# Kernel tuning notes

Measured on AMD Instinct MI355X. Metric: run time of the kernel, lower is better.

The kernel has to match this reference:

```python
import jax, jax.numpy as jnp
import numpy as np
from jax import lax


def ternarize(w):
    """Standard TWN ternarization with straight-through estimator.
    delta = 0.7*mean(|w|); alpha = mean(|w|) over kept entries; w_t = alpha*sign(w)*mask.
    """
    a = jnp.abs(w)
    delta = 0.7 * a.mean()
    mask = (a > delta).astype(w.dtype)
    alpha = (a * mask).sum() / jnp.maximum(mask.sum(), 1.0)
    wt = alpha * jnp.sign(w) * mask
    return w + lax.stop_gradient(wt - w)  # STE


def conv3x3(x, w, b):
    y = lax.conv_general_dilated(x, ternarize(w), window_strides=(1, 1),
                                 padding=((1, 1), (1, 1)),
                                 dimension_numbers=('NCHW', 'OIHW', 'NCHW'))
    return y + b[None, :, None, None]


def maxpool2(x):
    return lax.reduce_window(x, -jnp.inf, lax.max, (1, 1, 2, 2), (1, 1, 2, 2), 'VALID')


def setup_inputs() -> dict:
    key = jax.random.key(0)
    ks = jax.random.split(key, 11)
    s = lambda k, shape, scale: jax.random.normal(k, shape, dtype=jnp.float32) * scale
    return {
        'x':   s(ks[0], (1024, 3, 32, 32), 1.0),
        'w1':  s(ks[1], (64, 3, 3, 3), 0.1),
        'b1':  s(ks[2], (64,), 0.01),
        'w2':  s(ks[3], (128, 64, 3, 3), 0.05),
        'b2':  s(ks[4], (128,), 0.01),
        'w3':  s(ks[5], (256, 128, 3, 3), 0.03),
        'b3':  s(ks[6], (256,), 0.01),
        'wf1': s(ks[7], (256, 4096), 0.02),
        'bf1': s(ks[8], (256,), 0.01),
        'wf2': s(ks[9], (10, 256), 0.06),
        'bf2': s(ks[10], (10,), 0.01),
    }


def reference(x, w1, b1, w2, b2, w3, b3, wf1, bf1, wf2, bf2):
    x = maxpool2(jax.nn.relu(conv3x3(x, w1, b1)))   # [B,64,16,16]
    x = maxpool2(jax.nn.relu(conv3x3(x, w2, b2)))   # [B,128,8,8]
    x = maxpool2(jax.nn.relu(conv3x3(x, w3, b3)))   # [B,256,4,4]
    x = x.reshape(-1, 256 * 4 * 4)
    x = jax.nn.relu(x @ ternarize(wf1).T + bf1)     # [B,256]
    return x @ ternarize(wf2).T + bf2               # [B,10]
```

## Files before the change

### kernel.cpp

```cpp
#include <hip/hip_runtime.h>
#include <hip/hip_bf16.h>


typedef __attribute__((ext_vector_type(8))) short short8;
typedef __attribute__((ext_vector_type(4))) float f32x4;
typedef __attribute__((ext_vector_type(4))) int i32x4;

#define GLOAD_LDS16(g, l)                                              \
    __builtin_amdgcn_global_load_lds(                                  \
        (const __attribute__((address_space(1))) void*)(g),            \
        (__attribute__((address_space(3))) void*)(l), 16, 0, 0)

__device__ __forceinline__ unsigned short f2bf(float x) {
    unsigned u = __float_as_uint(x);
    return (unsigned short)((u + 0x7fffu + ((u >> 16) & 1u)) >> 16);
}
__device__ __forceinline__ float bf2f(unsigned short b) {
    return __uint_as_float(((unsigned)b) << 16);
}

__device__ __forceinline__ float calc_S1(const double* __restrict__ scr,
                                         float amaxx) {
    const int* ii = (const int*)(scr + 20);
    const double c2 = scr[2];
    const float alpha1 = (float)(scr[1] / (c2 > 1.0 ? c2 : 1.0));
    const float ub = alpha1 * (float)ii[3] * amaxx + __int_as_float(ii[6]);
    return 32512.0f / fmaxf(ub, 1e-30f);
}
__device__ __forceinline__ float calc_S2(const double* __restrict__ scr,
                                         float amax1) {
    const int* ii = (const int*)(scr + 20);
    const double c2 = scr[6];
    const float alpha2 = (float)(scr[5] / (c2 > 1.0 ? c2 : 1.0));
    const float ub = alpha2 * (float)ii[4] * amax1 + __int_as_float(ii[7]);
    return 32512.0f / fmaxf(ub, 1e-30f);
}
__device__ __forceinline__ float calc_S3(const double* __restrict__ scr,
                                         float amax2) {
    const int* ii = (const int*)(scr + 20);
    const double c2 = scr[10];
    const float alpha3 = (float)(scr[9] / (c2 > 1.0 ? c2 : 1.0));
    const float ub = alpha3 * (float)ii[5] * amax2 + __int_as_float(ii[8]);
    return 32512.0f / fmaxf(ub, 1e-30f);
}

#define WS_W1B   0
#define N_W1B    2048
#define WS_W2P   (WS_W1B + N_W1B)
#define N_W2P    (9*128*64)
#define WS_W3P   (WS_W2P + N_W2P)
#define N_W3P    (9*256*128)
#define WS_WTF1  (WS_W3P + N_W3P)
#define N_WTF1   (256*4096)
#define WS_WTF2  (WS_WTF1 + N_WTF1)
#define N_WTF2   (10*256)
#define WS_A1    (WS_WTF2 + N_WTF2)
#define N_A1     (1024*256*64)
#define WS_A2    (WS_A1 + N_A1)
#define N_A2     (1024*64*128)
#define WS_A3    (WS_A2 + N_A2)
#define N_A3     (1024*16*256)
#define WS_F1    (WS_A3 + N_A3)
#define N_F1     (1024*256)
#define WS_SCR   (WS_F1 + N_F1)

#define FC1_S    8

struct TernArgs {
    const float* w[6];
    int n[6];
};

__global__ void tern_stats1(TernArgs ta, double* __restrict__ scr) {
    const int wi = blockIdx.y;
    const float* __restrict__ w = ta.w[wi];
    const int n = ta.n[wi];
    __shared__ double red[4];
    const int lane = threadIdx.x & 63, wv = threadIdx.x >> 6;
    if (wi == 5) {
        float m = 0.f;
        for (int i = blockIdx.x * blockDim.x + threadIdx.x; i < n;
             i += gridDim.x * blockDim.x)
            m = fmaxf(m, fabsf(w[i]));
        #pragma unroll
        for (int off = 32; off > 0; off >>= 1)
            m = fmaxf(m, __shfl_down(m, off, 64));
        if (lane == 0) red[wv] = (double)m;
        __syncthreads();
        if (threadIdx.x == 0) {
            float mm = (float)fmax(fmax(red[0], red[1]), fmax(red[2], red[3]));
            atomicMax((int*)(scr + 20), __float_as_int(mm));
        }
        return;
    }
    double s = 0.0;
    for (int i = blockIdx.x * blockDim.x + threadIdx.x; i < n;
         i += gridDim.x * blockDim.x)
        s += (double)fabsf(w[i]);
    #pragma unroll
    for (int off = 32; off > 0; off >>= 1) s += __shfl_down(s, off, 64);
    if (lane == 0) red[wv] = s;
    __syncthreads();
    if (threadIdx.x == 0)
        atomicAdd(scr + wi * 4, red[0] + red[1] + red[2] + red[3]);
}

__global__ void tern_stats2(TernArgs ta,
                            const float* __restrict__ b1v,
                            const float* __restrict__ b2v,
                            const float* __restrict__ b3v,
                            signed char* __restrict__ w1b,
                            signed char* __restrict__ w2p8,
                            signed char* __restrict__ w3p8,
                            signed char* __restrict__ wtf1b8,
                            signed char* __restrict__ wtf2b8,
                            double* __restrict__ scr) {
    const int wi = blockIdx.y;
    const int lane = threadIdx.x & 63, wv = threadIdx.x >> 6;

    if (wi == 5) {
        int* ii = (int*)(scr + 20);
        const int gw = blockIdx.x * 4 + wv;
        if (gw < 64) {
            const float d = (float)(0.7 * scr[0] / 1728.0);
            const float* row = ta.w[0] + gw * 27;
            int c = (lane < 27) ? (fabsf(row[lane]) > d ? 1 : 0) : 0;
            #pragma unroll
            for (int off = 32; off > 0; off >>= 1)
                c += __shfl_down(c, off, 64);
            if (lane == 0) atomicMax(ii + 3, c);
        } else if (gw < 192) {
            const float d = (float)(0.7 * scr[4] / 73728.0);
            const float* row = ta.w[1] + (long)(gw - 64) * 576;
            int c = 0;
            for (int k = lane; k < 576; k += 64)
                c += (fabsf(row[k]) > d) ? 1 : 0;
            #pragma unroll
            for (int off = 32; off > 0; off >>= 1)
                c += __shfl_down(c, off, 64);
            if (lane == 0) atomicMax(ii + 4, c);
        } else if (gw < 448) {
            const float d = (float)(0.7 * scr[8] / 294912.0);
            const float* row = ta.w[2] + (long)(gw - 192) * 1152;
            int c = 0;
            for (int k = lane; k < 1152; k += 64)
                c += (fabsf(row[k]) > d) ? 1 : 0;
            #pragma unroll
            for (int off = 32; off > 0; off >>= 1)
                c += __shfl_down(c, off, 64);
            if (lane == 0) atomicMax(ii + 5, c);
        } else if (gw < 451) {
            const float* bv = (gw == 448) ? b1v : (gw == 449) ? b2v : b3v;
            const int nb = (gw == 448) ? 64 : (gw == 449) ? 128 : 256;
            float m = 0.f;
            for (int k = lane; k < nb; k += 64) m = fmaxf(m, fabsf(bv[k]));
            #pragma unroll
            for (int off = 32; off > 0; off >>= 1)
                m = fmaxf(m, __shfl_down(m, off, 64));
            if (lane == 0)
                atomicMax(ii + 6 + (gw - 448), __float_as_int(m));
        }
        return;
    }

    const float* __restrict__ w = ta.w[wi];
    const int n = ta.n[wi];
    const float delta = (float)(0.7 * scr[wi * 4] / (double)n);

    if (wi == 0) {
        const int z0 = blockIdx.x * blockDim.x + threadIdx.x;
        const int zstride = gridDim.x * blockDim.x;
        for (int i = z0; i < 8192; i += zstride) {
            const int k = i & 63;
            const int plane = i >> 12;
            const bool sign_slot = plane == 0 ? (k < 27)
                                              : (k >= 32 && k < 59);
            if (!sign_slot) w1b[i] = 0;
        }
    }

    double ms = 0.0, cnt = 0.0;
    for (int i = blockIdx.x * blockDim.x + threadIdx.x; i < n;
         i += gridDim.x * blockDim.x) {
        const float v = w[i];
        const float a = fabsf(v);
        const bool mk = (a > delta);
        if (mk) { ms += (double)a; cnt += 1.0; }
        const signed char s = mk ? (v > 0.0f ? 1 : -1) : 0;
        if (wi == 0) {
            const int co = i / 27;
            const int kp = i % 27;
            w1b[co * 64 + kp] = s;
            w1b[4096 + co * 64 + 32 + kp] = s;
        } else if (wi == 1 || wi == 2) {
            const int CIc = (wi == 1) ? 64 : 128;
            const int COc = (wi == 1) ? 128 : 256;
            signed char* dst = (wi == 1) ? w2p8 : w3p8;
            const int co = i / (CIc * 9);
            const int r = i % (CIc * 9);
            const int ci = r / 9, tap = r % 9;
            dst[(tap * COc + co) * CIc + ci] = s;
        } else if (wi == 3) {
            const int j = i >> 12;
            const int k = i & 4095;
            const int px = k & 15, c = k >> 4;
            wtf1b8[(long)j * 4096 + px * 256 + c] = s;
        } else {
            wtf2b8[i] = s;
        }
    }
    #pragma unroll
    for (int off = 32; off > 0; off >>= 1) {
        ms += __shfl_down(ms, off, 64);
        cnt += __shfl_down(cnt, off, 64);
    }
    __shared__ double redm[4], redc[4];
    if (lane == 0) { redm[wv] = ms; redc[wv] = cnt; }
    __syncthreads();
    if (threadIdx.x == 0) {
        atomicAdd(scr + wi * 4 + 1, redm[0] + redm[1] + redm[2] + redm[3]);
        atomicAdd(scr + wi * 4 + 2, redc[0] + redc[1] + redc[2] + redc[3]);
    }
}

__global__ __launch_bounds__(256) void conv1_i8(
        const float* __restrict__ x,
        const signed char* __restrict__ w1b,
        const float* __restrict__ bias,
        const double* __restrict__ scr,
        const int* __restrict__ amax_x,
        int* __restrict__ amax_out,
        signed char* __restrict__ a1q) {
    constexpr int PL = 3472;
    __shared__ __align__(16) char X[2 * PL];
    __shared__ float redm[4];

    const int b = blockIdx.x;
    const int tid = threadIdx.x;
    const float amx = fmaxf(__int_as_float(*amax_x), 1e-30f);
    const float S = 32512.0f / amx;
    const float S1 = calc_S1(scr, __int_as_float(*amax_x));

    for (int i = tid; i < 2 * PL / 16; i += 256)
        ((int4*)X)[i] = make_int4(0, 0, 0, 0);
    __syncthreads();

    for (int i = tid; i < 768; i += 256) {
        const float4 v = ((const float4*)(x + (long)b * 3072))[i];
        const int e = i * 4;
        const int ci = e >> 10;
        const int rem = e & 1023;
        const int h = rem >> 5, w = rem & 31;
        const int base = ci * 1156 + (h + 1) * 34 + (w + 1);
        const float f[4] = {v.x, v.y, v.z, v.w};
        #pragma unroll
        for (int j = 0; j < 4; j++) {
            const int q = __float2int_rn(f[j] * S);
            const int ql = (q << 24) >> 24;
            const int qh = (q - ql) >> 8;
            X[base + j] = (char)ql;
            X[PL + base + j] = (char)qh;
        }
    }
    __syncthreads();

    const int lane = tid & 63;
    const int wid = tid >> 6;
    const int lm = lane & 15;
    const int kg = lane >> 4;

    const int poff = (kg >= 2) ? PL : 0;
    int cst[16];
    #pragma unroll
    for (int j = 0; j < 16; j++) {
        const int kp = (kg & 1) * 16 + j;
        cst[j] = (kp < 27)
                     ? ((kp / 9) * 1156 + ((kp % 9) / 3) * 34 + (kp % 9) % 3)
                     : 0;
    }

    i32x4 BL[4], BH[4];
    #pragma unroll
    for (int nt = 0; nt < 4; nt++) {
        const int co = nt * 16 + lm;
        BL[nt] = *(const i32x4*)(w1b + (long)co * 64 + kg * 16);
        BH[nt] = *(const i32x4*)(w1b + 4096 + (long)co * 64 + kg * 16);
    }

    const double c2 = scr[2];
    const float alpha = (float)(scr[1] / (c2 > 1.0 ? c2 : 1.0));
    const float dq = alpha / S;
    float tmax = 0.f;
    signed char* yb = a1q + (long)b * 32768;

    for (int tt = 0; tt < 16; ++tt) {
        const int t = wid * 16 + tt;
        const int pp = t * 4 + (lm >> 2);
        const int sub = lm & 3;
        const int h = 2 * (pp >> 4) + (sub >> 1);
        const int w = 2 * (pp & 15) + (sub & 1);
        const int base = poff + h * 34 + w;
        unsigned d[4] = {0u, 0u, 0u, 0u};
        #pragma unroll
        for (int j = 0; j < 16; j++) {
            const unsigned byte = (unsigned char)X[base + cst[j]];
            d[j >> 2] |= byte << ((j & 3) * 8);
        }
        i32x4 Af;
        Af[0] = (int)d[0]; Af[1] = (int)d[1];
        Af[2] = (int)d[2]; Af[3] = (int)d[3];

        const int opp = t * 4 + kg;
        const int ho = opp >> 4, wo = opp & 15;
        signed char* yrow = yb + ((long)ho * 2048) + wo * 64;
        #pragma unroll
        for (int nt = 0; nt < 4; nt++) {
            i32x4 aL = 0, aH = 0;
            aL = __builtin_amdgcn_mfma_i32_16x16x64_i8(Af, BL[nt], aL, 0, 0, 0);
            aH = __builtin_amdgcn_mfma_i32_16x16x64_i8(Af, BH[nt], aH, 0, 0, 0);
            const int s0 = aH[0] * 256 + aL[0];
            const int s1 = aH[1] * 256 + aL[1];
            const int s2 = aH[2] * 256 + aL[2];
            const int s3 = aH[3] * 256 + aL[3];
            int sm = s0 > s1 ? s0 : s1;
            const int sn = s2 > s3 ? s2 : s3;
            sm = sm > sn ? sm : sn;
            const int co = nt * 16 + lm;
            const float o = fmaxf(dq * (float)sm + bias[co], 0.f);
            tmax = fmaxf(tmax, o);
            const int q = (int)(o * S1 + 0.5f);
            const int ql = (q << 24) >> 24;
            const int qh = (q + 128) >> 8;
            const int slot = (nt + ((wo + 1) >> 1) + 2 * (ho + 1)) & 3;
            const int off = slot * 16 + lm;
            yrow[off] = (char)ql;
            yrow[1024 + off] = (char)qh;
        }
    }

    #pragma unroll
    for (int off = 32; off > 0; off >>= 1)
        tmax = fmaxf(tmax, __shfl_down(tmax, off, 64));
    if (lane == 0) redm[wid] = tmax;
    __syncthreads();
    if (tid == 0) {
        float m = fmaxf(fmaxf(redm[0], redm[1]), fmaxf(redm[2], redm[3]));
        atomicMax(amax_out, __float_as_int(m));
    }
}

template <int CI, int HI, int CO, int HB, int WM, int WN, int MODE, int WIDX>
__global__ __launch_bounds__(256, 2) void conv_i8(
        const signed char* __restrict__ xin,
        const signed char* __restrict__ wp,
        const float* __restrict__ bias,
        const double* __restrict__ scr,
        const int* __restrict__ amax_x,
        const int* __restrict__ amax_1,
        int* __restrict__ amax_2,
        void* __restrict__ yout) {
    constexpr int CH8 = CI / 64;
    constexpr int NITER = 9 * CH8;
    constexpr int HR = HI / HB;
    constexpr int ROWS = HR + 2;
    constexpr int COLS = HI + 2;
    constexpr int NPIX = ROWS * COLS;
    constexpr int PSTR = NPIX * 64 + 32;
    constexpr int PO = HI / 2;
    constexpr int POR = HR / 2;
    constexpr int MT = 4, NT = 4;
    constexpr int NPL = 2 * CH8;
    constexpr int RWQ = HI * 64 * 2;
    static_assert(WM * WN == 4, "4 waves");
    static_assert(WM * 64 == HR * HI, "M covers slab pixels");
    static_assert(WN * 64 == CO, "N covers all co");
    static_assert(MODE != 0 || (CI == 64 && RWQ == 2048), "conv2 shape");
    static_assert(MODE != 1 || (CI == 128 && HB == 1), "conv3 shape");
    static_assert(HB <= 2, "row compaction assumes <=1 invalid row per end");
    static_assert((COLS & 1) == 0, "swizzle parity uses even COLS");

    __shared__ __align__(16) char X[NPL * PSTR];
    __shared__ __align__(16) char RAW2[(MODE == 1) ? 16384 : 16];
    __shared__ float redm[4];

    const int bimg = blockIdx.x / HB;
    const int hb = blockIdx.x % HB;
    const int tid = threadIdx.x;
    const int lane = tid & 63;
    const int wid = tid >> 6;

    const float S_in = (MODE == 0)
                           ? calc_S1(scr, __int_as_float(*amax_x))
                           : calc_S2(scr, __int_as_float(*amax_1));

    const int rlo = (hb == 0) ? 1 : 0;
    const int rhi = (hb == HB - 1) ? (ROWS - 1) : ROWS;

    if (MODE == 0) {
        for (int r = rlo; r < rhi; r++) {
            #pragma unroll
            for (int pl = 0; pl < 2; pl++) {
                if (wid == ((r * 2 + pl) & 3)) {
                    const int h = hb * HR + r - 1;
                    const signed char* src = xin +
                        (long)(bimg * HI + h) * RWQ + pl * 1024 + lane * 16;
                    GLOAD_LDS16(src, &X[pl * PSTR + (r * COLS + 1) * 64]);
                }
            }
        }
    } else {
        #pragma unroll
        for (int j = 0; j < 16; j++) {
            if (wid == (j & 3)) {
                const signed char* src = xin + (long)bimg * 16384 +
                                         j * 1024 + lane * 16;
                GLOAD_LDS16(src, &RAW2[j * 1024]);
            }
        }
    }

    {
        const int nfull = ((hb == 0) ? 1 : 0) + ((hb == HB - 1) ? 1 : 0);
        const int NP1 = ROWS * 2;
        const int NPZ = NP1 + nfull * (COLS - 2);
        for (int i = tid; i < NPZ * NPL * 4; i += 256) {
            const int u = i & 3;
            const int t = i >> 2;
            const int g = t % NPL;
            const int e = t / NPL;
            int p;
            if (e < NP1) {
                const int row = e >> 1;
                p = row * COLS + ((e & 1) ? (COLS - 1) : 0);
            } else {
                const int e2 = e - NP1;
                const int inFirst = (hb == 0) && (e2 < COLS - 2);
                const int fr = inFirst ? 0 : (ROWS - 1);
                const int cc = inFirst ? e2
                                       : (e2 - ((hb == 0) ? (COLS - 2) : 0));
                p = fr * COLS + 1 + cc;
            }
            *(int4*)&X[g * PSTR + p * 64 + u * 16] = make_int4(0, 0, 0, 0);
        }
    }

    if (MODE == 1) {
        __syncthreads();
        #pragma unroll
        for (int k = 0; k < 16; k++) {
            const int v = tid + k * 256;
            const int h = v >> 9;
            const int r = v & 511;
            const int g = r >> 7;
            const int b4 = (r & 127) << 2;
            const unsigned d = *(const unsigned*)&RAW2[v << 2];
            *(unsigned*)&X[g * PSTR + ((h + 1) * COLS + 1) * 64 + b4] = d;
        }
    }
    __syncthreads();

    const int wm = (WM == 1) ? 0 : (wid >> 1);
    const int wn = (WM == 1) ? wid : (wid & 1);
    const int lm = lane & 15;
    const int kg = lane >> 4;

    int pq[MT];
    #pragma unroll
    for (int mt = 0; mt < MT; mt++) {
        const int m = (wm * MT + mt) * 16 + lm;
        const int pp = m >> 2, sub = m & 3;
        const int lph = pp / PO, lpw = pp % PO;
        const int h = 2 * lph + (sub >> 1);
        const int w = 2 * lpw + (sub & 1);
        pq[mt] = ((h * COLS + w) << 6) | ((h & 1) << 3) | (w & 7);
    }
    const signed char* bp[NT];
    #pragma unroll
    for (int nt = 0; nt < NT; nt++) {
        const int co = (wn * NT + nt) * 16 + lm;
        bp[nt] = wp + (long)co * CI + kg * 16;
    }

    i32x4 accL[MT][NT], accH[MT][NT];
    #pragma unroll
    for (int mt = 0; mt < MT; mt++)
        #pragma unroll
        for (int nt = 0; nt < NT; nt++) { accL[mt][nt] = 0; accH[mt][nt] = 0; }

    i32x4 Bb[2][NT];
    #pragma unroll
    for (int nt = 0; nt < NT; nt++) Bb[0][nt] = *(const i32x4*)(bp[nt]);

    #pragma unroll 2
    for (int it = 0; it < NITER; ++it) {
        const int cur = it & 1, nxt = cur ^ 1;
        if (it + 1 < NITER) {
            const int it1 = it + 1;
            const int tap = it1 / CH8, ch1 = it1 % CH8;
            const int woff = tap * CO * CI + ch1 * 64;
            #pragma unroll
            for (int nt = 0; nt < NT; nt++)
                Bb[nxt][nt] = *(const i32x4*)(bp[nt] + woff);
        }
        const int tap = it / CH8, ch = it % CH8;
        const int ty = tap / 3, tx = tap % 3;
        const int DT = (ty * COLS + tx) << 6;
        const int typ = ty & 1;
        int ao[MT];
        #pragma unroll
        for (int mt = 0; mt < MT; mt++) {
            const int q = pq[mt];
            const int slot = (kg + ((((q >> 3) & 1) + typ) & 1) * 2 +
                              (((q & 7) + tx) >> 1)) & 3;
            ao[mt] = (q & ~63) + DT + (slot << 4);
        }
        {
            i32x4 Af[MT];
            #pragma unroll
            for (int mt = 0; mt < MT; mt++)
                Af[mt] = *(const i32x4*)&X[ch * PSTR + ao[mt]];
            #pragma unroll
            for (int mt = 0; mt < MT; mt++)
                #pragma unroll
                for (int nt = 0; nt < NT; nt++)
                    accL[mt][nt] = __builtin_amdgcn_mfma_i32_16x16x64_i8(
                        Af[mt], Bb[cur][nt], accL[mt][nt], 0, 0, 0);
        }
        {
            i32x4 Af[MT];
            #pragma unroll
            for (int mt = 0; mt < MT; mt++)
                Af[mt] = *(const i32x4*)&X[(CH8 + ch) * PSTR + ao[mt]];
            #pragma unroll
            for (int mt = 0; mt < MT; mt++)
                #pragma unroll
                for (int nt = 0; nt < NT; nt++)
                    accH[mt][nt] = __builtin_amdgcn_mfma_i32_16x16x64_i8(
                        Af[mt], Bb[cur][nt], accH[mt][nt], 0, 0, 0);
        }
    }

    const double* wst = scr + WIDX * 4;
    const double c2 = wst[2];
    const float alpha = (float)(wst[1] / (c2 > 1.0 ? c2 : 1.0));
    const float dq = alpha / S_in;
    if (MODE == 0) {
        const float S2 = calc_S2(scr, __int_as_float(*amax_1));
        signed char* oq = (signed char*)yout;
        float tmax = 0.f;
        #pragma unroll
        for (int mt = 0; mt < MT; mt++) {
            const int pp = (wm * MT + mt) * 4 + kg;
            const int lph = pp / PO, lpw = pp % PO;
            const int h = hb * POR + lph;
            const int w = lpw;
            #pragma unroll
            for (int nt = 0; nt < NT; nt++) {
                const int co2 = (wn * NT + nt) * 16 + lm;
                const i32x4 aL = accL[mt][nt], aH = accH[mt][nt];
                int s0 = aH[0] * 256 + aL[0];
                int s1 = aH[1] * 256 + aL[1];
                int s2 = aH[2] * 256 + aL[2];
                int s3 = aH[3] * 256 + aL[3];
                int sm = s0 > s1 ? s0 : s1;
                int sn = s2 > s3 ? s2 : s3;
                sm = sm > sn ? sm : sn;
                const float o = fmaxf(dq * (float)sm + bias[co2], 0.f);
                tmax = fmaxf(tmax, o);
                const int q = (int)(o * S2 + 0.5f);
                const int ql = (q << 24) >> 24;
                const int qh = (q + 128) >> 8;
                const int slot = (((co2 >> 4) & 3) + ((w + 1) >> 1) +
                                  2 * (h + 1)) & 3;
                const long base = (long)bimg * 16384 + h * 2048 +
                                  (co2 >> 6) * 512 + w * 64 + slot * 16 +
                                  (co2 & 15);
                oq[base] = (char)ql;
                oq[base + 1024] = (char)qh;
            }
        }
        #pragma unroll
        for (int off = 32; off > 0; off >>= 1)
            tmax = fmaxf(tmax, __shfl_down(tmax, off, 64));
        if (lane == 0) redm[wid] = tmax;
        __syncthreads();
        if (tid == 0) {
            float m = fmaxf(fmaxf(redm[0], redm[1]), fmaxf(redm[2], redm[3]));
            atomicMax(amax_2, __float_as_int(m));
        }
    } else {
        const float S3 = calc_S3(scr, __int_as_float(*amax_2));
        signed char* oq = (signed char*)yout;
        #pragma unroll
        for (int mt = 0; mt < MT; mt++) {
            const int pp = (wm * MT + mt) * 4 + kg;
            const int lph = pp / PO, lpw = pp % PO;
            const int gpp = (hb * POR + lph) * PO + lpw;
            signed char* yr = oq + (long)bimg * 8192 + gpp * 512;
            #pragma unroll
            for (int nt = 0; nt < NT; nt++) {
                const int co = (wn * NT + nt) * 16 + lm;
                const i32x4 aL = accL[mt][nt], aH = accH[mt][nt];
                int s0 = aH[0] * 256 + aL[0];
                int s1 = aH[1] * 256 + aL[1];
                int s2 = aH[2] * 256 + aL[2];
                int s3 = aH[3] * 256 + aL[3];
                int sm = s0 > s1 ? s0 : s1;
                int sn = s2 > s3 ? s2 : s3;
                sm = sm > sn ? sm : sn;
                const float o = fmaxf(dq * (float)sm + bias[co], 0.f);
                const int q = (int)(o * S3 + 0.5f);
                const int ql = (q << 24) >> 24;
                const int qh = (q + 128) >> 8;
                yr[co] = (char)ql;
                yr[256 + co] = (char)qh;
            }
        }
    }
}

template <int S>
__global__ __launch_bounds__(256) void fc1_i8(
        const signed char* __restrict__ A,
        const signed char* __restrict__ Bw,
        float* __restrict__ parts) {
    constexpr int KCH = 4096 / S;
    constexpr int NCH = KCH / 64;
    const int m0 = blockIdx.x * 64;
    const int n0 = blockIdx.y * 64;
    const int s = blockIdx.z;
    const int tid = threadIdx.x;
    const int lane = tid & 63, wid = tid >> 6;
    const int wm = wid >> 1, wn = wid & 1;
    const int lm = lane & 15, kg = lane >> 4;

    const int k0 = s * KCH;
    const signed char* ap[2];
    const signed char* bp[2];
    #pragma unroll
    for (int t = 0; t < 2; t++) {
        ap[t] = A + (long)(m0 + wm * 32 + t * 16 + lm) * 8192;
        bp[t] = Bw + (long)(n0 + wn * 32 + t * 16 + lm) * 4096 + k0 + kg * 16;
    }

    i32x4 accL[2][2], accH[2][2];
    #pragma unroll
    for (int mt = 0; mt < 2; mt++)
        #pragma unroll
        for (int nt = 0; nt < 2; nt++) { accL[mt][nt] = 0; accH[mt][nt] = 0; }

    #pragma unroll
    for (int ch = 0; ch < NCH; ++ch) {
        const int kb = k0 + ch * 64;
        const int aoff = (kb >> 8) * 512 + (kb & 255) + kg * 16;
        i32x4 Ah[2], Al[2], Bb[2];
        #pragma unroll
        for (int t = 0; t < 2; t++) {
            Al[t] = *(const i32x4*)(ap[t] + aoff);
            Ah[t] = *(const i32x4*)(ap[t] + aoff + 256);
            Bb[t] = *(const i32x4*)(bp[t] + ch * 64);
        }
        #pragma unroll
        for (int mt = 0; mt < 2; mt++)
            #pragma unroll
            for (int nt = 0; nt < 2; nt++) {
                accH[mt][nt] = __builtin_amdgcn_mfma_i32_16x16x64_i8(
                    Ah[mt], Bb[nt], accH[mt][nt], 0, 0, 0);
                accL[mt][nt] = __builtin_amdgcn_mfma_i32_16x16x64_i8(
                    Al[mt], Bb[nt], accL[mt][nt], 0, 0, 0);
            }
    }

    #pragma unroll
    for (int mt = 0; mt < 2; mt++) {
        #pragma unroll
        for (int r = 0; r < 4; r++) {
            const int b = m0 + wm * 32 + mt * 16 + kg * 4 + r;
            #pragma unroll
            for (int nt = 0; nt < 2; nt++) {
                const int j = n0 + wn * 32 + nt * 16 + lm;
                const int sum = accH[mt][nt][r] * 256 + accL[mt][nt][r];
                parts[((long)s * 1024 + b) * 256 + j] = (float)sum;
            }
        }
    }
}

template <int S>
__global__ __launch_bounds__(256) void fc2_fused(
        const float* __restrict__ parts,
        const double* __restrict__ scr,
        const int* __restrict__ amax_2,
        const float* __restrict__ bf1v,
        const signed char* __restrict__ wtf2b8,
        const float* __restrict__ bf2v,
        float* __restrict__ out) {
    __shared__ float sf[256];
    const int b = blockIdx.x;
    const int j = threadIdx.x;
    float s = 0.f;
    #pragma unroll
    for (int p = 0; p < S; p++)
        s += parts[(long)p * 262144 + (long)b * 256 + j];
    const double c2 = scr[14];
    const float alpha = (float)(scr[13] / (c2 > 1.0 ? c2 : 1.0));
    const float S3 = calc_S3(scr, __int_as_float(*amax_2));
    sf[j] = fmaxf(alpha * s / S3 + bf1v[j], 0.f);
    __syncthreads();
    const double c4 = scr[18];
    const float alpha4 = (float)(scr[17] / (c4 > 1.0 ? c4 : 1.0));
    const int lane = threadIdx.x & 63, wid = threadIdx.x >> 6;
    for (int k = wid; k < 10; k += 4) {
        const signed char* wr = wtf2b8 + k * 256;
        float acc = 0.f;
        #pragma unroll
        for (int t = 0; t < 4; t++)
            acc += sf[lane + t * 64] * (float)wr[lane + t * 64];
        #pragma unroll
        for (int off = 32; off > 0; off >>= 1)
            acc += __shfl_down(acc, off, 64);
        if (lane == 0) out[(long)b * 10 + k] = acc * alpha4 + bf2v[k];
    }
}

extern "C" void kernel_launch(void* const* d_in, const int* in_sizes, int n_in,
                              void* d_out, int out_size, void* d_ws, size_t ws_size,
                              hipStream_t stream) {
    const float* x   = (const float*)d_in[0];
    const float* w1  = (const float*)d_in[1];
    const float* b1  = (const float*)d_in[2];
    const float* w2  = (const float*)d_in[3];
    const float* b2  = (const float*)d_in[4];
    const float* w3  = (const float*)d_in[5];
    const float* b3  = (const float*)d_in[6];
    const float* wf1 = (const float*)d_in[7];
    const float* bf1 = (const float*)d_in[8];
    const float* wf2 = (const float*)d_in[9];
    const float* bf2 = (const float*)d_in[10];
    float* out = (float*)d_out;
    float* ws = (float*)d_ws;

    const int B = 1024;

    signed char*    w1b    = (signed char*)(ws + WS_W1B);
    signed char*    w2p8   = (signed char*)(ws + WS_W2P);
    signed char*    w3p8   = (signed char*)(ws + WS_W3P);
    signed char*    wtf1b8 = (signed char*)(ws + WS_WTF1);
    signed char*    wtf2b8 = (signed char*)(ws + WS_WTF2);
    signed char*    a1q    = (signed char*)(ws + WS_A1);
    signed char*    a2q    = (signed char*)(ws + WS_A2);
    signed char*    a3q    = (signed char*)(ws + WS_A3);
    double*         scr    = (double*)(ws + WS_SCR);
    int*            iscr   = (int*)(scr + 20);
    int*            amaxx  = iscr;
    int*            amax1  = iscr + 1;
    int*            amax2  = iscr + 2;
    float*          parts  = ws + WS_A1;

    hipMemsetAsync(scr, 0, 26 * sizeof(double), stream);

    TernArgs ta;
    ta.w[0] = w1;  ta.n[0] = 64 * 27;
    ta.w[1] = w2;  ta.n[1] = 128 * 64 * 9;
    ta.w[2] = w3;  ta.n[2] = 256 * 128 * 9;
    ta.w[3] = wf1; ta.n[3] = 256 * 4096;
    ta.w[4] = wf2; ta.n[4] = 10 * 256;
    ta.w[5] = x;   ta.n[5] = 1024 * 3 * 32 * 32;

    hipLaunchKernelGGL(tern_stats1, dim3(128, 6), dim3(256), 0, stream, ta, scr);
    hipLaunchKernelGGL(tern_stats2, dim3(128, 6), dim3(256), 0, stream,
                       ta, b1, b2, b3, w1b, w2p8, w3p8, wtf1b8, wtf2b8, scr);

    hipLaunchKernelGGL(conv1_i8, dim3(B), dim3(256), 0, stream,
                       x, w1b, b1, scr, amaxx, amax1, a1q);

    hipLaunchKernelGGL((conv_i8<64, 16, 128, 2, 2, 2, 0, 1>), dim3(B * 2),
                       dim3(256), 0, stream, a1q, w2p8, b2, scr, amaxx,
                       amax1, amax2, a2q);

    hipLaunchKernelGGL((conv_i8<128, 8, 256, 1, 1, 4, 1, 2>), dim3(B),
                       dim3(256), 0, stream, a2q, w3p8, b3, scr, amaxx,
                       amax1, amax2, a3q);

    hipLaunchKernelGGL((fc1_i8<FC1_S>), dim3(16, 4, FC1_S), dim3(256), 0, stream,
                       a3q, wtf1b8, parts);

    hipLaunchKernelGGL((fc2_fused<FC1_S>), dim3(B), dim3(256), 0, stream,
                       parts, scr, amax2, bf1, wtf2b8, bf2, out);
}
```

Baseline: 261.1 us.

## Fuse conv1 and conv2 into one kernel keeping conv1 output in LDS

Merges the conv1 and conv2 kernels so each block computes the pooled conv1 output for one image straight into shared-memory slabs. Conv2 then runs over two row halves from LDS, so the int8 activation no longer makes a round trip through global memory and one launch is dropped. Because conv2's input scale now has to be known before the conv1 max is reduced, it is derived from an analytic bound (calc_S2b) rather than the measured conv1 max. That may coarsen quantization. The fused kernel uses more LDS per block and does conv2 with half the blocks of before, which could reduce occupancy and parallelism.

```diff
diff --git a/kernel.cpp b/kernel.cpp
--- a/kernel.cpp
+++ b/kernel.cpp
@@ -27,13 +27,16 @@
     const float ub = alpha1 * (float)ii[3] * amaxx + __int_as_float(ii[6]);
     return 32512.0f / fmaxf(ub, 1e-30f);
 }
-__device__ __forceinline__ float calc_S2(const double* __restrict__ scr,
-                                         float amax1) {
+__device__ __forceinline__ float calc_S2b(const double* __restrict__ scr,
+                                          float amaxx) {
     const int* ii = (const int*)(scr + 20);
+    const double c1 = scr[2];
+    const float alpha1 = (float)(scr[1] / (c1 > 1.0 ? c1 : 1.0));
+    const float ub1 = alpha1 * (float)ii[3] * amaxx + __int_as_float(ii[6]);
     const double c2 = scr[6];
     const float alpha2 = (float)(scr[5] / (c2 > 1.0 ? c2 : 1.0));
-    const float ub = alpha2 * (float)ii[4] * amax1 + __int_as_float(ii[7]);
-    return 32512.0f / fmaxf(ub, 1e-30f);
+    const float ub2 = alpha2 * (float)ii[4] * ub1 + __int_as_float(ii[7]);
+    return 32512.0f / fmaxf(ub2, 1e-30f);
 }
 __device__ __forceinline__ float calc_S3(const double* __restrict__ scr,
                                          float amax2) {
@@ -223,26 +226,58 @@
     }
 }
 
-__global__ __launch_bounds__(256) void conv1_i8(
+__global__ __launch_bounds__(256, 2) void conv12_i8(
         const float* __restrict__ x,
         const signed char* __restrict__ w1b,
-        const float* __restrict__ bias,
+        const float* __restrict__ b1v,
+        const signed char* __restrict__ w2p,
+        const float* __restrict__ b2v,
         const double* __restrict__ scr,
         const int* __restrict__ amax_x,
-        int* __restrict__ amax_out,
-        signed char* __restrict__ a1q) {
+        int* __restrict__ amax_2,
+        signed char* __restrict__ a2q) {
     constexpr int PL = 3472;
-    __shared__ __align__(16) char X[2 * PL];
-    __shared__ float redm[4];
+    constexpr int COLS = 18;
+    constexpr int PSTR2 = 180 * 64 + 32;
+    constexpr int SLAB = 2 * PSTR2;
+    constexpr int PO = 8, POR = 4;
+    constexpr int MT = 4, NT = 4, CI = 64, CO = 128;
+
+    __shared__ __align__(16) char XA[2 * PL];
+    __shared__ __align__(16) char X2[2 * SLAB];
+    __shared__ float redt[4];
 
     const int b = blockIdx.x;
     const int tid = threadIdx.x;
+    const int lane = tid & 63, wid = tid >> 6;
+    const int lm = lane & 15, kg = lane >> 4;
+
     const float amx = fmaxf(__int_as_float(*amax_x), 1e-30f);
     const float S = 32512.0f / amx;
     const float S1 = calc_S1(scr, __int_as_float(*amax_x));
 
+    if (tid < 4) redt[tid] = 0.f;
     for (int i = tid; i < 2 * PL / 16; i += 256)
-        ((int4*)X)[i] = make_int4(0, 0, 0, 0);
+        ((int4*)XA)[i] = make_int4(0, 0, 0, 0);
+    for (int i = tid; i < 2 * 36 * 2 * 4; i += 256) {
+        const int u = i & 3;
+        const int t = i >> 2;
+        const int g = t & 1;
+        const int e = t >> 1;
+        const int slab = e / 36;
+        const int k = e % 36;
+        int p;
+        if (slab == 0)
+            p = (k < 18) ? k
+                         : ((1 + ((k - 18) >> 1)) * COLS +
+                            (((k - 18) & 1) ? (COLS - 1) : 0));
+        else
+            p = (k < 18) ? (9 * COLS + k)
+                         : ((((k - 18) >> 1)) * COLS +
+                            (((k - 18) & 1) ? (COLS - 1) : 0));
+        *(int4*)&X2[slab * SLAB + g * PSTR2 + p * 64 + u * 16] =
+            make_int4(0, 0, 0, 0);
+    }
     __syncthreads();
 
     for (int i = tid; i < 768; i += 256) {
@@ -258,212 +293,95 @@
             const int q = __float2int_rn(f[j] * S);
             const int ql = (q << 24) >> 24;
             const int qh = (q - ql) >> 8;
-            X[base + j] = (char)ql;
-            X[PL + base + j] = (char)qh;
+            XA[base + j] = (char)ql;
+            XA[PL + base + j] = (char)qh;
         }
     }
     __syncthreads();
 
-    const int lane = tid & 63;
-    const int wid = tid >> 6;
-    const int lm = lane & 15;
-    const int kg = lane >> 4;
-
-    const int poff = (kg >= 2) ? PL : 0;
-    int cst[16];
-    #pragma unroll
-    for (int j = 0; j < 16; j++) {
-        const int kp = (kg & 1) * 16 + j;
-        cst[j] = (kp < 27)
-                     ? ((kp / 9) * 1156 + ((kp % 9) / 3) * 34 + (kp % 9) % 3)
-                     : 0;
-    }
-
-    i32x4 BL[4], BH[4];
-    #pragma unroll
-    for (int nt = 0; nt < 4; nt++) {
-        const int co = nt * 16 + lm;
-        BL[nt] = *(const i32x4*)(w1b + (long)co * 64 + kg * 16);
-        BH[nt] = *(const i32x4*)(w1b + 4096 + (long)co * 64 + kg * 16);
-    }
-
-    const double c2 = scr[2];
-    const float alpha = (float)(scr[1] / (c2 > 1.0 ? c2 : 1.0));
-    const float dq = alpha / S;
-    float tmax = 0.f;
-    signed char* yb = a1q + (long)b * 32768;
-
-    for (int tt = 0; tt < 16; ++tt) {
-        const int t = wid * 16 + tt;
-        const int pp = t * 4 + (lm >> 2);
-        const int sub = lm & 3;
-        const int h = 2 * (pp >> 4) + (sub >> 1);
-        const int w = 2 * (pp & 15) + (sub & 1);
-        const int base = poff + h * 34 + w;
-        unsigned d[4] = {0u, 0u, 0u, 0u};
+    {
+        const int poff = (kg >= 2) ? PL : 0;
+        int cst[16];
         #pragma unroll
         for (int j = 0; j < 16; j++) {
-            const unsigned byte = (unsigned char)X[base + cst[j]];
-            d[j >> 2] |= byte << ((j & 3) * 8);
-        }
-        i32x4 Af;
-        Af[0] = (int)d[0]; Af[1] = (int)d[1];
-        Af[2] = (int)d[2]; Af[3] = (int)d[3];
-
-        const int opp = t * 4 + kg;
-        const int ho = opp >> 4, wo = opp & 15;
-        signed char* yrow = yb + ((long)ho * 2048) + wo * 64;
+            const int kp = (kg & 1) * 16 + j;
+            cst[j] = (kp < 27)
+                         ? ((kp / 9) * 1156 + ((kp % 9) / 3) * 34 +
+                            (kp % 9) % 3)
+                         : 0;
+        }
+        i32x4 BL[4], BH[4];
         #pragma unroll
         for (int nt = 0; nt < 4; nt++) {
-            i32x4 aL = 0, aH = 0;
-            aL = __builtin_amdgcn_mfma_i32_16x16x64_i8(Af, BL[nt], aL, 0, 0, 0);
-            aH = __builtin_amdgcn_mfma_i32_16x16x64_i8(Af, BH[nt], aH, 0, 0, 0);
-            const int s0 = aH[0] * 256 + aL[0];
-            const int s1 = aH[1] * 256 + aL[1];
-            const int s2 = aH[2] * 256 + aL[2];
-            const int s3 = aH[3] * 256 + aL[3];
-            int sm = s0 > s1 ? s0 : s1;
-            const int sn = s2 > s3 ? s2 : s3;
-            sm = sm > sn ? sm : sn;
             const int co = nt * 16 + lm;
-            const float o = fmaxf(dq * (float)sm + bias[co], 0.f);
-            tmax = fmaxf(tmax, o);
-            const int q = (int)(o * S1 + 0.5f);
-            const int ql = (q << 24) >> 24;
-            const int qh = (q + 128) >> 8;
-            const int slot = (nt + ((wo + 1) >> 1) + 2 * (ho + 1)) & 3;
-            const int off = slot * 16 + lm;
-            yrow[off] = (char)ql;
-            yrow[1024 + off] = (char)qh;
-        }
-    }
-
-    #pragma unroll
-    for (int off = 32; off > 0; off >>= 1)
-        tmax = fmaxf(tmax, __shfl_down(tmax, off, 64));
-    if (lane == 0) redm[wid] = tmax;
+            BL[nt] = *(const i32x4*)(w1b + (long)co * 64 + kg * 16);
+            BH[nt] = *(const i32x4*)(w1b + 4096 + (long)co * 64 + kg * 16);
+        }
+        const double c2a = scr[2];
+        const float alpha1 = (float)(scr[1] / (c2a > 1.0 ? c2a : 1.0));
+        const float dq1 = alpha1 / S;
+
+        for (int tt = 0; tt < 16; ++tt) {
+            const int t = wid * 16 + tt;
+            const int pp = t * 4 + (lm >> 2);
+            const int sub = lm & 3;
+            const int h = 2 * (pp >> 4) + (sub >> 1);
+            const int w = 2 * (pp & 15) + (sub & 1);
+            const int base = poff + h * 34 + w;
+            unsigned d[4] = {0u, 0u, 0u, 0u};
+            #pragma unroll
+            for (int j = 0; j < 16; j++) {
+                const unsigned byte = (unsigned char)XA[base + cst[j]];
+                d[j >> 2] |= byte << ((j & 3) * 8);
+            }
+            i32x4 Af;
+            Af[0] = (int)d[0]; Af[1] = (int)d[1];
+            Af[2] = (int)d[2]; Af[3] = (int)d[3];
+
+            const int opp = t * 4 + kg;
+            const int ho = opp >> 4, wo = opp & 15;
+            const int col = wo + 1;
+            #pragma unroll
+            for (int nt = 0; nt < 4; nt++) {
+                i32x4 aL = 0, aH = 0;
+                aL = __builtin_amdgcn_mfma_i32_16x16x64_i8(Af, BL[nt], aL,
+                                                           0, 0, 0);
+                aH = __builtin_amdgcn_mfma_i32_16x16x64_i8(Af, BH[nt], aH,
+                                                           0, 0, 0);
+                const int s0 = aH[0] * 256 + aL[0];
+                const int s1 = aH[1] * 256 + aL[1];
+                const int s2 = aH[2] * 256 + aL[2];
+                const int s3 = aH[3] * 256 + aL[3];
+                int sm = s0 > s1 ? s0 : s1;
+                const int sn = s2 > s3 ? s2 : s3;
+                sm = sm > sn ? sm : sn;
+                const int co = nt * 16 + lm;
+                const float o = fmaxf(dq1 * (float)sm + b1v[co], 0.f);
+                const int q = (int)(o * S1 + 0.5f);
+                const signed char ql = (signed char)((q << 24) >> 24);
+                const signed char qh = (signed char)((q + 128) >> 8);
+                const int sb = nt + (col >> 1);
+                if (ho <= 8) {
+                    const int r = ho + 1;
+                    const int slot = (sb + 2 * r) & 3;
+                    const int off = (r * COLS + col) * 64 + slot * 16 + lm;
+                    X2[off] = ql;
+                    X2[PSTR2 + off] = qh;
+                }
+                if (ho >= 7) {
+                    const int r = ho - 7;
+                    const int slot = (sb + 2 * r) & 3;
+                    const int off = (r * COLS + col) * 64 + slot * 16 + lm;
+                    X2[SLAB + off] = ql;
+                    X2[SLAB + PSTR2 + off] = qh;
+                }
+            }
+        }
+    }
     __syncthreads();
-    if (tid == 0) {
-        float m = fmaxf(fmaxf(redm[0], redm[1]), fmaxf(redm[2], redm[3]));
-        atomicMax(amax_out, __float_as_int(m));
-    }
-}
-
-template <int CI, int HI, int CO, int HB, int WM, int WN, int MODE, int WIDX>
-__global__ __launch_bounds__(256, 2) void conv_i8(
-        const signed char* __restrict__ xin,
-        const signed char* __restrict__ wp,
-        const float* __restrict__ bias,
-        const double* __restrict__ scr,
-        const int* __restrict__ amax_x,
-        const int* __restrict__ amax_1,
-        int* __restrict__ amax_2,
-        void* __restrict__ yout) {
-    constexpr int CH8 = CI / 64;
-    constexpr int NITER = 9 * CH8;
-    constexpr int HR = HI / HB;
-    constexpr int ROWS = HR + 2;
-    constexpr int COLS = HI + 2;
-    constexpr int NPIX = ROWS * COLS;
-    constexpr int PSTR = NPIX * 64 + 32;
-    constexpr int PO = HI / 2;
-    constexpr int POR = HR / 2;
-    constexpr int MT = 4, NT = 4;
-    constexpr int NPL = 2 * CH8;
-    constexpr int RWQ = HI * 64 * 2;
-    static_assert(WM * WN == 4, "4 waves");
-    static_assert(WM * 64 == HR * HI, "M covers slab pixels");
-    static_assert(WN * 64 == CO, "N covers all co");
-    static_assert(MODE != 0 || (CI == 64 && RWQ == 2048), "conv2 shape");
-    static_assert(MODE != 1 || (CI == 128 && HB == 1), "conv3 shape");
-    static_assert(HB <= 2, "row compaction assumes <=1 invalid row per end");
-    static_assert((COLS & 1) == 0, "swizzle parity uses even COLS");
-
-    __shared__ __align__(16) char X[NPL * PSTR];
-    __shared__ __align__(16) char RAW2[(MODE == 1) ? 16384 : 16];
-    __shared__ float redm[4];
-
-    const int bimg = blockIdx.x / HB;
-    const int hb = blockIdx.x % HB;
-    const int tid = threadIdx.x;
-    const int lane = tid & 63;
-    const int wid = tid >> 6;
-
-    const float S_in = (MODE == 0)
-                           ? calc_S1(scr, __int_as_float(*amax_x))
-                           : calc_S2(scr, __int_as_float(*amax_1));
-
-    const int rlo = (hb == 0) ? 1 : 0;
-    const int rhi = (hb == HB - 1) ? (ROWS - 1) : ROWS;
-
-    if (MODE == 0) {
-        for (int r = rlo; r < rhi; r++) {
-            #pragma unroll
-            for (int pl = 0; pl < 2; pl++) {
-                if (wid == ((r * 2 + pl) & 3)) {
-                    const int h = hb * HR + r - 1;
-                    const signed char* src = xin +
-                        (long)(bimg * HI + h) * RWQ + pl * 1024 + lane * 16;
-                    GLOAD_LDS16(src, &X[pl * PSTR + (r * COLS + 1) * 64]);
-                }
-            }
-        }
-    } else {
-        #pragma unroll
-        for (int j = 0; j < 16; j++) {
-            if (wid == (j & 3)) {
-                const signed char* src = xin + (long)bimg * 16384 +
-                                         j * 1024 + lane * 16;
-                GLOAD_LDS16(src, &RAW2[j * 1024]);
-            }
-        }
-    }
-
-    {
-        const int nfull = ((hb == 0) ? 1 : 0) + ((hb == HB - 1) ? 1 : 0);
-        const int NP1 = ROWS * 2;
-        const int NPZ = NP1 + nfull * (COLS - 2);
-        for (int i = tid; i < NPZ * NPL * 4; i += 256) {
-            const int u = i & 3;
-            const int t = i >> 2;
-            const int g = t % NPL;
-            const int e = t / NPL;
-            int p;
-            if (e < NP1) {
-                const int row = e >> 1;
-                p = row * COLS + ((e & 1) ? (COLS - 1) : 0);
-            } else {
-                const int e2 = e - NP1;
-                const int inFirst = (hb == 0) && (e2 < COLS - 2);
-                const int fr = inFirst ? 0 : (ROWS - 1);
-                const int cc = inFirst ? e2
-                                       : (e2 - ((hb == 0) ? (COLS - 2) : 0));
-                p = fr * COLS + 1 + cc;
-            }
-            *(int4*)&X[g * PSTR + p * 64 + u * 16] = make_int4(0, 0, 0, 0);
-        }
-    }
-
-    if (MODE == 1) {
-        __syncthreads();
-        #pragma unroll
-        for (int k = 0; k < 16; k++) {
-            const int v = tid + k * 256;
-            const int h = v >> 9;
-            const int r = v & 511;
-            const int g = r >> 7;
-            const int b4 = (r & 127) << 2;
-            const unsigned d = *(const unsigned*)&RAW2[v << 2];
-            *(unsigned*)&X[g * PSTR + ((h + 1) * COLS + 1) * 64 + b4] = d;
-        }
-    }
-    __syncthreads();
-
-    const int wm = (WM == 1) ? 0 : (wid >> 1);
-    const int wn = (WM == 1) ? wid : (wid & 1);
-    const int lm = lane & 15;
-    const int kg = lane >> 4;
-
+
+    const int wm = wid >> 1;
+    const int wn = wid & 1;
     int pq[MT];
     #pragma unroll
     for (int mt = 0; mt < MT; mt++) {
@@ -478,75 +396,73 @@
     #pragma unroll
     for (int nt = 0; nt < NT; nt++) {
         const int co = (wn * NT + nt) * 16 + lm;
-        bp[nt] = wp + (long)co * CI + kg * 16;
-    }
-
-    i32x4 accL[MT][NT], accH[MT][NT];
-    #pragma unroll
-    for (int mt = 0; mt < MT; mt++)
-        #pragma unroll
-        for (int nt = 0; nt < NT; nt++) { accL[mt][nt] = 0; accH[mt][nt] = 0; }
-
-    i32x4 Bb[2][NT];
-    #pragma unroll
-    for (int nt = 0; nt < NT; nt++) Bb[0][nt] = *(const i32x4*)(bp[nt]);
-
-    #pragma unroll 2
-    for (int it = 0; it < NITER; ++it) {
-        const int cur = it & 1, nxt = cur ^ 1;
-        if (it + 1 < NITER) {
-            const int it1 = it + 1;
-            const int tap = it1 / CH8, ch1 = it1 % CH8;
-            const int woff = tap * CO * CI + ch1 * 64;
-            #pragma unroll
-            for (int nt = 0; nt < NT; nt++)
-                Bb[nxt][nt] = *(const i32x4*)(bp[nt] + woff);
-        }
-        const int tap = it / CH8, ch = it % CH8;
-        const int ty = tap / 3, tx = tap % 3;
-        const int DT = (ty * COLS + tx) << 6;
-        const int typ = ty & 1;
-        int ao[MT];
-        #pragma unroll
-        for (int mt = 0; mt < MT; mt++) {
-            const int q = pq[mt];
-            const int slot = (kg + ((((q >> 3) & 1) + typ) & 1) * 2 +
-                              (((q & 7) + tx) >> 1)) & 3;
-            ao[mt] = (q & ~63) + DT + (slot << 4);
-        }
-        {
-            i32x4 Af[MT];
-            #pragma unroll
-            for (int mt = 0; mt < MT; mt++)
-                Af[mt] = *(const i32x4*)&X[ch * PSTR + ao[mt]];
-            #pragma unroll
-            for (int mt = 0; mt < MT; mt++)
+        bp[nt] = w2p + (long)co * CI + kg * 16;
+    }
+
+    for (int hb = 0; hb < 2; ++hb) {
+        const char* Xs = X2 + hb * SLAB;
+
+        i32x4 accL[MT][NT], accH[MT][NT];
+        #pragma unroll
+        for (int mt = 0; mt < MT; mt++)
+            #pragma unroll
+            for (int nt = 0; nt < NT; nt++) {
+                accL[mt][nt] = 0; accH[mt][nt] = 0;
+            }
+        i32x4 Bb[2][NT];
+        #pragma unroll
+        for (int nt = 0; nt < NT; nt++) Bb[0][nt] = *(const i32x4*)(bp[nt]);
+
+        #pragma unroll 2
+        for (int it = 0; it < 9; ++it) {
+            const int cur = it & 1, nxt = cur ^ 1;
+            if (it + 1 < 9) {
+                const int woff = (it + 1) * CO * CI;
                 #pragma unroll
                 for (int nt = 0; nt < NT; nt++)
-                    accL[mt][nt] = __builtin_amdgcn_mfma_i32_16x16x64_i8(
-                        Af[mt], Bb[cur][nt], accL[mt][nt], 0, 0, 0);
-        }
-        {
-            i32x4 Af[MT];
-            #pragma unroll
-            for (int mt = 0; mt < MT; mt++)
-                Af[mt] = *(const i32x4*)&X[(CH8 + ch) * PSTR + ao[mt]];
-            #pragma unroll
-            for (int mt = 0; mt < MT; mt++)
+                    Bb[nxt][nt] = *(const i32x4*)(bp[nt] + woff);
+            }
+            const int ty = it / 3, tx = it % 3;
+            const int DT = (ty * COLS + tx) << 6;
+            const int typ = ty & 1;
+            int ao[MT];
+            #pragma unroll
+            for (int mt = 0; mt < MT; mt++) {
+                const int q = pq[mt];
+                const int slot = (kg + ((((q >> 3) & 1) + typ) & 1) * 2 +
+                                  (((q & 7) + tx) >> 1)) & 3;
+                ao[mt] = (q & ~63) + DT + (slot << 4);
+            }
+            {
+                i32x4 Af[MT];
                 #pragma unroll
-                for (int nt = 0; nt < NT; nt++)
-                    accH[mt][nt] = __builtin_amdgcn_mfma_i32_16x16x64_i8(
-                        Af[mt], Bb[cur][nt], accH[mt][nt], 0, 0, 0);
-        }
-    }
-
-    const double* wst = scr + WIDX * 4;
-    const double c2 = wst[2];
-    const float alpha = (float)(wst[1] / (c2 > 1.0 ? c2 : 1.0));
-    const float dq = alpha / S_in;
-    if (MODE == 0) {
-        const float S2 = calc_S2(scr, __int_as_float(*amax_1));
-        signed char* oq = (signed char*)yout;
+                for (int mt = 0; mt < MT; mt++)
+                    Af[mt] = *(const i32x4*)&Xs[ao[mt]];
+                #pragma unroll
+                for (int mt = 0; mt < MT; mt++)
+                    #pragma unroll
+                    for (int nt = 0; nt < NT; nt++)
+                        accL[mt][nt] = __builtin_amdgcn_mfma_i32_16x16x64_i8(
+                            Af[mt], Bb[cur][nt], accL[mt][nt], 0, 0, 0);
+            }
+            {
+                i32x4 Af[MT];
+                #pragma unroll
+                for (int mt = 0; mt < MT; mt++)
+                    Af[mt] = *(const i32x4*)&Xs[PSTR2 + ao[mt]];
+                #pragma unroll
+                for (int mt = 0; mt < MT; mt++)
+                    #pragma unroll
+                    for (int nt = 0; nt < NT; nt++)
+                        accH[mt][nt] = __builtin_amdgcn_mfma_i32_16x16x64_i8(
+                            Af[mt], Bb[cur][nt], accH[mt][nt], 0, 0, 0);
+            }
+        }
+
+        const double c2b = scr[6];
+        const float alpha2 = (float)(scr[5] / (c2b > 1.0 ? c2b : 1.0));
+        const float dq2 = alpha2 / S1;
+        const float S2p = calc_S2b(scr, __int_as_float(*amax_x));
         float tmax = 0.f;
         #pragma unroll
         for (int mt = 0; mt < MT; mt++) {
@@ -565,56 +481,208 @@
                 int sm = s0 > s1 ? s0 : s1;
                 int sn = s2 > s3 ? s2 : s3;
                 sm = sm > sn ? sm : sn;
-                const float o = fmaxf(dq * (float)sm + bias[co2], 0.f);
+                const float o = fmaxf(dq2 * (float)sm + b2v[co2], 0.f);
                 tmax = fmaxf(tmax, o);
-                const int q = (int)(o * S2 + 0.5f);
+                const int q = (int)(o * S2p + 0.5f);
                 const int ql = (q << 24) >> 24;
                 const int qh = (q + 128) >> 8;
                 const int slot = (((co2 >> 4) & 3) + ((w + 1) >> 1) +
                                   2 * (h + 1)) & 3;
-                const long base = (long)bimg * 16384 + h * 2048 +
+                const long base = (long)b * 16384 + h * 2048 +
                                   (co2 >> 6) * 512 + w * 64 + slot * 16 +
                                   (co2 & 15);
-                oq[base] = (char)ql;
-                oq[base + 1024] = (char)qh;
+                a2q[base] = (char)ql;
+                a2q[base + 1024] = (char)qh;
             }
         }
         #pragma unroll
         for (int off = 32; off > 0; off >>= 1)
             tmax = fmaxf(tmax, __shfl_down(tmax, off, 64));
-        if (lane == 0) redm[wid] = tmax;
-        __syncthreads();
-        if (tid == 0) {
-            float m = fmaxf(fmaxf(redm[0], redm[1]), fmaxf(redm[2], redm[3]));
-            atomicMax(amax_2, __float_as_int(m));
-        }
-    } else {
-        const float S3 = calc_S3(scr, __int_as_float(*amax_2));
-        signed char* oq = (signed char*)yout;
+        if (lane == 0) redt[wid] = fmaxf(redt[wid], tmax);
+    }
+    __syncthreads();
+    if (tid == 0) {
+        float m = fmaxf(fmaxf(redt[0], redt[1]), fmaxf(redt[2], redt[3]));
+        atomicMax(amax_2, __float_as_int(m));
+    }
+}
+
+__global__ __launch_bounds__(256, 2) void conv3_i8(
+        const signed char* __restrict__ xin,
+        const signed char* __restrict__ wp,
+        const float* __restrict__ bias,
+        const double* __restrict__ scr,
+        const int* __restrict__ amax_x,
+        const int* __restrict__ amax_2,
+        signed char* __restrict__ a3q) {
+    constexpr int CI = 128, HI = 8, CO = 256;
+    constexpr int CH8 = CI / 64;
+    constexpr int NITER = 9 * CH8;
+    constexpr int ROWS = HI + 2, COLS = HI + 2;
+    constexpr int NPIX = ROWS * COLS;
+    constexpr int PSTR = NPIX * 64 + 32;
+    constexpr int PO = HI / 2;
+    constexpr int MT = 4, NT = 4;
+    constexpr int NPL = 2 * CH8;
+
+    __shared__ __align__(16) char X[NPL * PSTR];
+    __shared__ __align__(16) char RAW2[16384];
+
+    const int bimg = blockIdx.x;
+    const int tid = threadIdx.x;
+    const int lane = tid & 63;
+    const int wid = tid >> 6;
+
+    const float S_in = calc_S2b(scr, __int_as_float(*amax_x));
+
+    #pragma unroll
+    for (int j = 0; j < 16; j++) {
+        if (wid == (j & 3)) {
+            const signed char* src = xin + (long)bimg * 16384 +
+                                     j * 1024 + lane * 16;
+            GLOAD_LDS16(src, &RAW2[j * 1024]);
+        }
+    }
+
+    {
+        constexpr int NPZ = 2 * COLS + 2 * (ROWS - 2);
+        for (int i = tid; i < NPZ * NPL * 4; i += 256) {
+            const int u = i & 3;
+            const int t = i >> 2;
+            const int g = t % NPL;
+            const int e = t / NPL;
+            int p;
+            if (e < COLS) p = e;
+            else if (e < 2 * COLS) p = (ROWS - 1) * COLS + (e - COLS);
+            else {
+                const int e2 = e - 2 * COLS;
+                p = (1 + (e2 >> 1)) * COLS + ((e2 & 1) ? (COLS - 1) : 0);
+            }
+            *(int4*)&X[g * PSTR + p * 64 + u * 16] = make_int4(0, 0, 0, 0);
+        }
+    }
+
+    __syncthreads();
+    #pragma unroll
+    for (int k = 0; k < 16; k++) {
+        const int v = tid + k * 256;
+        const int h = v >> 9;
+        const int r = v & 511;
+        const int g = r >> 7;
+        const int b4 = (r & 127) << 2;
+        const unsigned d = *(const unsigned*)&RAW2[v << 2];
+        *(unsigned*)&X[g * PSTR + ((h + 1) * COLS + 1) * 64 + b4] = d;
+    }
+    __syncthreads();
+
+    const int wm = 0;
+    const int wn = wid;
+    const int lm = lane & 15;
+    const int kg = lane >> 4;
+
+    int pq[MT];
+    #pragma unroll
+    for (int mt = 0; mt < MT; mt++) {
+        const int m = (wm * MT + mt) * 16 + lm;
+        const int pp = m >> 2, sub = m & 3;
+        const int lph = pp / PO, lpw = pp % PO;
+        const int h = 2 * lph + (sub >> 1);
+        const int w = 2 * lpw + (sub & 1);
+        pq[mt] = ((h * COLS + w) << 6) | ((h & 1) << 3) | (w & 7);
+    }
+    const signed char* bp[NT];
+    #pragma unroll
+    for (int nt = 0; nt < NT; nt++) {
+        const int co = (wn * NT + nt) * 16 + lm;
+        bp[nt] = wp + (long)co * CI + kg * 16;
+    }
+
+    i32x4 accL[MT][NT], accH[MT][NT];
+    #pragma unroll
+    for (int mt = 0; mt < MT; mt++)
+        #pragma unroll
+        for (int nt = 0; nt < NT; nt++) { accL[mt][nt] = 0; accH[mt][nt] = 0; }
+
+    i32x4 Bb[2][NT];
+    #pragma unroll
+    for (int nt = 0; nt < NT; nt++) Bb[0][nt] = *(const i32x4*)(bp[nt]);
+
+    #pragma unroll 2
+    for (int it = 0; it < NITER; ++it) {
+        const int cur = it & 1, nxt = cur ^ 1;
+        if (it + 1 < NITER) {
+            const int it1 = it + 1;
+            const int tap = it1 / CH8, ch1 = it1 % CH8;
+            const int woff = tap * CO * CI + ch1 * 64;
+            #pragma unroll
+            for (int nt = 0; nt < NT; nt++)
+                Bb[nxt][nt] = *(const i32x4*)(bp[nt] + woff);
+        }
+        const int tap = it / CH8, ch = it % CH8;
+        const int ty = tap / 3, tx = tap % 3;
+        const int DT = (ty * COLS + tx) << 6;
+        const int typ = ty & 1;
+        int ao[MT];
         #pragma unroll
         for (int mt = 0; mt < MT; mt++) {
-            const int pp = (wm * MT + mt) * 4 + kg;
-            const int lph = pp / PO, lpw = pp % PO;
-            const int gpp = (hb * POR + lph) * PO + lpw;
-            signed char* yr = oq + (long)bimg * 8192 + gpp * 512;
-            #pragma unroll
-            for (int nt = 0; nt < NT; nt++) {
-                const int co = (wn * NT + nt) * 16 + lm;
-                const i32x4 aL = accL[mt][nt], aH = accH[mt][nt];
-                int s0 = aH[0] * 256 + aL[0];
-                int s1 = aH[1] * 256 + aL[1];
-                int s2 = aH[2] * 256 + aL[2];
-                int s3 = aH[3] * 256 + aL[3];
-                int sm = s0 > s1 ? s0 : s1;
-                int sn = s2 > s3 ? s2 : s3;
-                sm = sm > sn ? sm : sn;
-                const float o = fmaxf(dq * (float)sm + bias[co], 0.f);
-                const int q = (int)(o * S3 + 0.5f);
-                const int ql = (q << 24) >> 24;
-                const int qh = (q + 128) >> 8;
-                yr[co] = (char)ql;
-                yr[256 + co] = (char)qh;
-            }
+            const int q = pq[mt];
+            const int slot = (kg + ((((q >> 3) & 1) + typ) & 1) * 2 +
+                              (((q & 7) + tx) >> 1)) & 3;
+            ao[mt] = (q & ~63) + DT + (slot << 4);
+        }
+        {
+            i32x4 Af[MT];
+            #pragma unroll
+            for (int mt = 0; mt < MT; mt++)
+                Af[mt] = *(const i32x4*)&X[ch * PSTR + ao[mt]];
+            #pragma unroll
+            for (int mt = 0; mt < MT; mt++)
+                #pragma unroll
+                for (int nt = 0; nt < NT; nt++)
+                    accL[mt][nt] = __builtin_amdgcn_mfma_i32_16x16x64_i8(
+                        Af[mt], Bb[cur][nt], accL[mt][nt], 0, 0, 0);
+        }
+        {
+            i32x4 Af[MT];
+            #pragma unroll
+            for (int mt = 0; mt < MT; mt++)
+                Af[mt] = *(const i32x4*)&X[(CH8 + ch) * PSTR + ao[mt]];
+            #pragma unroll
+            for (int mt = 0; mt < MT; mt++)
+                #pragma unroll
+                for (int nt = 0; nt < NT; nt++)
+                    accH[mt][nt] = __builtin_amdgcn_mfma_i32_16x16x64_i8(
+                        Af[mt], Bb[cur][nt], accH[mt][nt], 0, 0, 0);
+        }
+    }
+
+    const double c2 = scr[10];
+    const float alpha = (float)(scr[9] / (c2 > 1.0 ? c2 : 1.0));
+    const float dq = alpha / S_in;
+    const float S3 = calc_S3(scr, __int_as_float(*amax_2));
+    #pragma unroll
+    for (int mt = 0; mt < MT; mt++) {
+        const int pp = (wm * MT + mt) * 4 + kg;
+        const int lph = pp / PO, lpw = pp % PO;
+        const int gpp = lph * PO + lpw;
+        signed char* yr = a3q + (long)bimg * 8192 + gpp * 512;
+        #pragma unroll
+        for (int nt = 0; nt < NT; nt++) {
+            const int co = (wn * NT + nt) * 16 + lm;
+            const i32x4 aL = accL[mt][nt], aH = accH[mt][nt];
+            int s0 = aH[0] * 256 + aL[0];
+            int s1 = aH[1] * 256 + aL[1];
+            int s2 = aH[2] * 256 + aL[2];
+            int s3 = aH[3] * 256 + aL[3];
+            int sm = s0 > s1 ? s0 : s1;
+            int sn = s2 > s3 ? s2 : s3;
+            sm = sm > sn ? sm : sn;
+            const float o = fmaxf(dq * (float)sm + bias[co], 0.f);
+            const int q = (int)(o * S3 + 0.5f);
+            const int ql = (q << 24) >> 24;
+            const int qh = (q + 128) >> 8;
+            yr[co] = (char)ql;
+            yr[256 + co] = (char)qh;
         }
     }
 }
@@ -747,13 +815,11 @@
     signed char*    w3p8   = (signed char*)(ws + WS_W3P);
     signed char*    wtf1b8 = (signed char*)(ws + WS_WTF1);
     signed char*    wtf2b8 = (signed char*)(ws + WS_WTF2);
-    signed char*    a1q    = (signed char*)(ws + WS_A1);
     signed char*    a2q    = (signed char*)(ws + WS_A2);
     signed char*    a3q    = (signed char*)(ws + WS_A3);
     double*         scr    = (double*)(ws + WS_SCR);
     int*            iscr   = (int*)(scr + 20);
     int*            amaxx  = iscr;
-    int*            amax1  = iscr + 1;
     int*            amax2  = iscr + 2;
     float*          parts  = ws + WS_A1;
 
@@ -771,16 +837,11 @@
     hipLaunchKernelGGL(tern_stats2, dim3(128, 6), dim3(256), 0, stream,
                        ta, b1, b2, b3, w1b, w2p8, w3p8, wtf1b8, wtf2b8, scr);
 
-    hipLaunchKernelGGL(conv1_i8, dim3(B), dim3(256), 0, stream,
-                       x, w1b, b1, scr, amaxx, amax1, a1q);
-
-    hipLaunchKernelGGL((conv_i8<64, 16, 128, 2, 2, 2, 0, 1>), dim3(B * 2),
-                       dim3(256), 0, stream, a1q, w2p8, b2, scr, amaxx,
-                       amax1, amax2, a2q);
-
-    hipLaunchKernelGGL((conv_i8<128, 8, 256, 1, 1, 4, 1, 2>), dim3(B),
-                       dim3(256), 0, stream, a2q, w3p8, b3, scr, amaxx,
-                       amax1, amax2, a3q);
+    hipLaunchKernelGGL(conv12_i8, dim3(B), dim3(256), 0, stream,
+                       x, w1b, b1, w2p8, b2, scr, amaxx, amax2, a2q);
+
+    hipLaunchKernelGGL(conv3_i8, dim3(B), dim3(256), 0, stream,
+                       a2q, w3p8, b3, scr, amaxx, amax2, a3q);
 
     hipLaunchKernelGGL((fc1_i8<FC1_S>), dim3(16, 4, FC1_S), dim3(256), 0, stream,
                        a3q, wtf1b8, parts);
```

Result: slower. 319.6 us (+22.4%).
